# Optimization experiments

Measured on AMD Instinct MI355X. Metric: run time of the kernel, lower is better.

The kernel has to match this reference:

```python
import jax, jax.numpy as jnp
import numpy as np


def _chamfer(samp_pc, ref_pc):
    """Squared-L2 chamfer: returns (cost_p1_p2 [B,N], cost_p2_p1 [B,M]).

    samp_pc: [B, N, 3], ref_pc: [B, M, 3]
    """
    s2 = jnp.sum(samp_pc * samp_pc, axis=-1)  # [B, N]
    r2 = jnp.sum(ref_pc * ref_pc, axis=-1)    # [B, M]
    cross = jnp.einsum('bnd,bmd->bnm', samp_pc, ref_pc)  # [B, N, M]
    d2 = s2[:, :, None] + r2[:, None, :] - 2.0 * cross   # [B, N, M]
    d2 = jnp.maximum(d2, 0.0)  # numerical floor
    cost_p1_p2 = jnp.min(d2, axis=2)  # [B, N] nearest ref for each samp point
    cost_p2_p1 = jnp.min(d2, axis=1)  # [B, M] nearest samp for each ref point
    return cost_p1_p2, cost_p2_p1


def setup_inputs() -> dict:
    key = jax.random.key(0)
    k1, k2 = jax.random.split(key)
    B, N, M = 16, 2048, 8192
    ref_pc = jax.random.normal(k1, (B, M, 3), dtype=jnp.float32)
    samp_pc = jax.random.normal(k2, (B, N, 3), dtype=jnp.float32)
    return {"ref_pc": ref_pc, "samp_pc": samp_pc}


def reference(ref_pc, samp_pc):
    cost_p1_p2, cost_p2_p1 = _chamfer(samp_pc, ref_pc)
    cd_p = (jnp.sqrt(cost_p1_p2).mean(axis=1) + jnp.sqrt(cost_p2_p1).mean(axis=1)) / 2.0
    cd_t = cost_p1_p2.mean(axis=1) + cost_p2_p1.mean(axis=1)
    return (cd_p, cd_t)
```

## Files before the change

kernel.cpp:

```cpp
#include <hip/hip_runtime.h>
#include <math.h>

#define BB 16
#define NN 2048
#define MM 8192

#define BLK 256
#define QSTG 512
#define NSTAGE (NN / QSTG)
#define CTS (QSTG / 32)

typedef __attribute__((ext_vector_type(8))) short short8;
typedef __attribute__((ext_vector_type(16))) float f32x16;

union U16 { uint4 u; short8 s; };

static __device__ __forceinline__ unsigned short f2bf(float f) {
    unsigned int u = __float_as_uint(f);
    unsigned int r = (u + 0x7FFFu + ((u >> 16) & 1u)) >> 16;
    return (unsigned short)r;
}
static __device__ __forceinline__ float bf2f(unsigned short h) {
    return __uint_as_float(((unsigned int)h) << 16);
}

static __device__ __forceinline__ void glds16(const uint4* g, uint4* l) {
    __builtin_amdgcn_global_load_lds(
        (const __attribute__((address_space(1))) unsigned int*)g,
        (__attribute__((address_space(3))) unsigned int*)l,
        16, 0, 0);
}

#define DPP_MIN(v, CTRL)                                                      \
    v = fminf(v, __uint_as_float((unsigned)__builtin_amdgcn_update_dpp(       \
                     0, (int)__float_as_uint(v), CTRL, 0xF, 0xF, true)))
#define SWZ16_MIN(v)                                                          \
    v = fminf(v, __uint_as_float((unsigned)__builtin_amdgcn_ds_swizzle(       \
                     (int)__float_as_uint(v), 0x401F)))


__global__ void __launch_bounds__(BLK) prep_kernel(const float* __restrict__ ref,
                                                   const float* __restrict__ samp,
                                                   unsigned short* __restrict__ Qpk,
                                                   unsigned short* __restrict__ Rpk,
                                                   unsigned int* __restrict__ ws1) {
    const int i = blockIdx.x * BLK + threadIdx.x;
    const int PN = BB * NN;
    float a5[5];
    unsigned short h[3][5];
    unsigned short K[32];

    if (i < PN) {
        const float* s0 = samp + (size_t)i * 3;
        float x = s0[0], y = s0[1], z = s0[2];
        a5[0] = x; a5[1] = y; a5[2] = z;
        a5[3] = 1.f; a5[4] = fmaf(x, x, fmaf(y, y, z * z));
#pragma unroll
        for (int j = 0; j < 5; ++j) {
            float v = a5[j];
            h[0][j] = f2bf(v); float r1 = v - bf2f(h[0][j]);
            h[1][j] = f2bf(r1); float r2 = r1 - bf2f(h[1][j]);
            h[2][j] = f2bf(r2);
        }
        const int ordQ[6] = {0, 1, 0, 2, 0, 1};
#pragma unroll
        for (int f = 0; f < 2; ++f) {
#pragma unroll
            for (int p2 = 0; p2 < 3; ++p2)
#pragma unroll
                for (int j2 = 0; j2 < 5; ++j2)
                    K[f * 16 + p2 * 5 + j2] = h[ordQ[f * 3 + p2]][j2];
            K[f * 16 + 15] = 0;
        }
        unsigned int uu[16];
#pragma unroll
        for (int t = 0; t < 16; ++t)
            uu[t] = (unsigned int)K[2 * t] | ((unsigned int)K[2 * t + 1] << 16);
        uint4 c0 = make_uint4(uu[0], uu[1], uu[2], uu[3]);
        uint4 c1 = make_uint4(uu[4], uu[5], uu[6], uu[7]);
        uint4 c2 = make_uint4(uu[8], uu[9], uu[10], uu[11]);
        uint4 c3 = make_uint4(uu[12], uu[13], uu[14], uu[15]);
        uint4* dst = (uint4*)(Qpk + (size_t)i * 32);
        const int sw = (i >> 1) & 3;
        dst[0 ^ sw] = c0; dst[1 ^ sw] = c1; dst[2 ^ sw] = c2; dst[3 ^ sw] = c3;
        ws1[i] = 0x7F7F7F7Fu;
    } else if (i < PN + BB * MM) {
        const int j = i - PN;
        const float* r0 = ref + (size_t)j * 3;
        float x = r0[0], y = r0[1], z = r0[2];
        a5[0] = -2.f * x; a5[1] = -2.f * y; a5[2] = -2.f * z;
        a5[3] = fmaf(x, x, fmaf(y, y, z * z)); a5[4] = 1.f;
#pragma unroll
        for (int jj = 0; jj < 5; ++jj) {
            float v = a5[jj];
            h[0][jj] = f2bf(v); float r1 = v - bf2f(h[0][jj]);
            h[1][jj] = f2bf(r1); float r2 = r1 - bf2f(h[1][jj]);
            h[2][jj] = f2bf(r2);
        }
        const int ordR[6] = {0, 0, 1, 0, 2, 1};
#pragma unroll
        for (int f = 0; f < 2; ++f) {
#pragma unroll
            for (int p2 = 0; p2 < 3; ++p2)
#pragma unroll
                for (int j2 = 0; j2 < 5; ++j2)
                    K[f * 16 + p2 * 5 + j2] = h[ordR[f * 3 + p2]][j2];
            K[f * 16 + 15] = 0;
        }
        unsigned int uu[16];
#pragma unroll
        for (int t = 0; t < 16; ++t)
            uu[t] = (unsigned int)K[2 * t] | ((unsigned int)K[2 * t + 1] << 16);
        uint4* dst = (uint4*)(Rpk + (size_t)j * 32);
        dst[0] = make_uint4(uu[0], uu[1], uu[2], uu[3]);
        dst[1] = make_uint4(uu[4], uu[5], uu[6], uu[7]);
        dst[2] = make_uint4(uu[8], uu[9], uu[10], uu[11]);
        dst[3] = make_uint4(uu[12], uu[13], uu[14], uu[15]);
    }
}

__global__ void __launch_bounds__(BLK, 4) sweep_kernel(const unsigned short* __restrict__ Qpk,
                                                       const unsigned short* __restrict__ Rpk,
                                                       float* __restrict__ ws2,
                                                       unsigned int* __restrict__ ws1) {
    __shared__ uint4 Qt[2][QSTG * 4];
    __shared__ unsigned int qMin[NN];

    const int b = blockIdx.x;
    const int m0 = blockIdx.y * 256;
    const int tid = threadIdx.x;
    const int w = tid >> 6;
    const int l = tid & 63;
    const int p = l & 31;
    const int kh = l >> 5;

    const uint4* R4 = (const uint4*)Rpk + ((size_t)(b * MM + m0 + w * 64 + p)) * 4;
    U16 a0f0, a0f1, a1f0, a1f1;
    a0f0.u = R4[kh];        a0f1.u = R4[2 + kh];
    a1f0.u = R4[128 + kh];  a1f1.u = R4[128 + 2 + kh];

    for (int i = tid; i < NN; i += BLK) qMin[i] = 0x7F7F7F7Fu;

    const uint4* Q4 = (const uint4*)Qpk + (size_t)b * (NN * 4);
    {
        uint4* dst = &Qt[0][0];
#pragma unroll
        for (int k = 0; k < 8; ++k) glds16(Q4 + k * BLK + tid, dst + k * BLK + tid);
    }
    __syncthreads();

    float run0[16], run1[16];
#pragma unroll
    for (int j = 0; j < 16; ++j) { run0[j] = INFINITY; run1[j] = INFINITY; }

    const int sw = (p >> 1) & 3;
    const f32x16 fz = {0.f, 0.f, 0.f, 0.f, 0.f, 0.f, 0.f, 0.f,
                       0.f, 0.f, 0.f, 0.f, 0.f, 0.f, 0.f, 0.f};

    for (int st = 0; st < NSTAGE; ++st) {
        const uint4* qb = &Qt[st & 1][0];
        if (st < NSTAGE - 1) {
            const uint4* src = Q4 + (size_t)(st + 1) * (QSTG * 4);
            uint4* dst = &Qt[(st + 1) & 1][0];
#pragma unroll
            for (int k = 0; k < 8; ++k) glds16(src + k * BLK + tid, dst + k * BLK + tid);
        }
#pragma unroll 2
        for (int ct = 0; ct < CTS; ++ct) {
            const int pg = (ct * 32 + p) * 4;
            U16 b0, b1;
            b0.u = qb[pg + (kh ^ sw)];
            b1.u = qb[pg + ((2 + kh) ^ sw)];
            f32x16 d0 = __builtin_amdgcn_mfma_f32_32x32x16_bf16(a0f0.s, b0.s, fz, 0, 0, 0);
            d0 = __builtin_amdgcn_mfma_f32_32x32x16_bf16(a0f1.s, b1.s, d0, 0, 0, 0);
            f32x16 d1 = __builtin_amdgcn_mfma_f32_32x32x16_bf16(a1f0.s, b0.s, fz, 0, 0, 0);
            d1 = __builtin_amdgcn_mfma_f32_32x32x16_bf16(a1f1.s, b1.s, d1, 0, 0, 0);
#pragma unroll
            for (int j = 0; j < 16; ++j) {
                run0[j] = fminf(run0[j], d0[j]);
                run1[j] = fminf(run1[j], d1[j]);
            }
            float tv[8];
#pragma unroll
            for (int k = 0; k < 8; ++k) tv[k] = fminf(d0[k], d0[k + 8]);
#pragma unroll
            for (int k = 0; k < 8; ++k) tv[k] = fminf(tv[k], fminf(d1[k], d1[k + 8]));
#pragma unroll
            for (int k = 0; k < 4; ++k) tv[k] = fminf(tv[k], tv[k + 4]);
            float t = fminf(fminf(tv[0], tv[2]), fminf(tv[1], tv[3]));
            atomicMin(&qMin[st * QSTG + ct * 32 + p], __float_as_uint(fmaxf(t, 0.f)));
        }
        __syncthreads();
    }

#pragma unroll
    for (int i = tid; i < NN; i += BLK)
        atomicMin(&ws1[(size_t)b * NN + i], qMin[i]);

#pragma unroll
    for (int j = 0; j < 16; ++j) {
        DPP_MIN(run0[j], 0xB1);  DPP_MIN(run0[j], 0x4E);
        DPP_MIN(run0[j], 0x141); DPP_MIN(run0[j], 0x140);
        SWZ16_MIN(run0[j]);
        DPP_MIN(run1[j], 0xB1);  DPP_MIN(run1[j], 0x4E);
        DPP_MIN(run1[j], 0x141); DPP_MIN(run1[j], 0x140);
        SWZ16_MIN(run1[j]);
    }
    float out = 0.f;
#pragma unroll
    for (int j = 0; j < 16; ++j) { if (p == j)      out = run0[j]; }
#pragma unroll
    for (int j = 0; j < 16; ++j) { if (p == 16 + j) out = run1[j]; }
    const int t2 = p >> 4, j4 = p & 15;
    const int row = t2 * 32 + (j4 & 3) + ((j4 >> 2) << 3) + 4 * kh;
    ws2[(size_t)b * MM + m0 + w * 64 + row] = fmaxf(out, 0.f);
}

#define BLKR 1024
__global__ void __launch_bounds__(BLKR) reduce_kernel(const unsigned int* __restrict__ ws1,
                                                      const float* __restrict__ ws2,
                                                      float* __restrict__ out) {
    const int b = blockIdx.x;
    const int tid = threadIdx.x;
    const int lane = tid & 63;
    const int wv = tid >> 6;

    float sd1 = 0.f, sr1 = 0.f, sd2 = 0.f, sr2 = 0.f;
#pragma unroll
    for (int i = tid; i < NN; i += BLKR) {
        float v = __uint_as_float(ws1[(size_t)b * NN + i]);
        sd1 += v;
        sr1 += sqrtf(v);
    }
#pragma unroll
    for (int i = tid; i < MM; i += BLKR) {
        float v = ws2[(size_t)b * MM + i];
        sd2 += v;
        sr2 += sqrtf(v);
    }
#pragma unroll
    for (int s = 32; s > 0; s >>= 1) {
        sd1 += __shfl_xor(sd1, s);
        sr1 += __shfl_xor(sr1, s);
        sd2 += __shfl_xor(sd2, s);
        sr2 += __shfl_xor(sr2, s);
    }

    __shared__ float4 red[BLKR / 64];
    if (lane == 0) red[wv] = make_float4(sd1, sr1, sd2, sr2);
    __syncthreads();
    if (tid == 0) {
        float4 acc = red[0];
#pragma unroll
        for (int w = 1; w < BLKR / 64; ++w) {
            acc.x += red[w].x; acc.y += red[w].y;
            acc.z += red[w].z; acc.w += red[w].w;
        }
        out[b]      = (acc.y * (1.0f / NN) + acc.w * (1.0f / MM)) * 0.5f;
        out[BB + b] = acc.x * (1.0f / NN) + acc.z * (1.0f / MM);
    }
}

extern "C" void kernel_launch(void* const* d_in, const int* in_sizes, int n_in,
                              void* d_out, int out_size, void* d_ws, size_t ws_size,
                              hipStream_t stream) {
    const float* ref  = (const float*)d_in[0];
    const float* samp = (const float*)d_in[1];
    float* out = (float*)d_out;

    float* ws2 = (float*)d_ws;
    unsigned int* ws1 = (unsigned int*)(ws2 + (size_t)BB * MM);
    unsigned short* Qpk = (unsigned short*)(ws1 + (size_t)BB * NN);
    unsigned short* Rpk = Qpk + (size_t)BB * NN * 32;

    const int P = BB * (NN + MM);
    prep_kernel<<<P / BLK, BLK, 0, stream>>>(ref, samp, Qpk, Rpk, ws1);

    dim3 gs(BB, MM / 256);
    sweep_kernel<<<gs, BLK, 0, stream>>>(Qpk, Rpk, ws2, ws1);

    reduce_kernel<<<BB, BLKR, 0, stream>>>(ws1, ws2, out);
}
```

Baseline: 96.32 us.

## Split query dimension across blocks, fuse ref packing into sweep, drop global atomics

Adds a third grid dimension that splits the sample points into two halves, doubling the number of sweep blocks and halving the per-block LDS stage size. The reference-point bf16 packing moves from the prep kernel into the sweep kernel, where it is staged through shared memory. This removes the Rpk global round trip. Per-block column minima are written to a partial buffer instead of using global atomicMin, and the reduce kernel takes the min across the partials. The cost is more partial-buffer traffic in the reduce and redundant ref packing, since each of the two z-blocks repacks the same ref points.

Result: faster. 89.18 us (-7.4%).

```diff
diff --git a/kernel.cpp b/kernel.cpp
--- a/kernel.cpp
+++ b/kernel.cpp
@@ -6,9 +6,12 @@
 #define MM 8192
 
 #define BLK 256
-#define QSTG 512
-#define NSTAGE (NN / QSTG)
+#define QSPL 2
+#define NQ (NN / QSPL)
+#define QSTG 256
+#define NSTAGE (NQ / QSTG)
 #define CTS (QSTG / 32)
+#define YB (MM / 256)
 
 typedef __attribute__((ext_vector_type(8))) short short8;
 typedef __attribute__((ext_vector_type(16))) float f32x16;
@@ -39,22 +42,68 @@
                      (int)__float_as_uint(v), 0x401F)))
 
 
-__global__ void __launch_bounds__(BLK) prep_kernel(const float* __restrict__ ref,
-                                                   const float* __restrict__ samp,
-                                                   unsigned short* __restrict__ Qpk,
-                                                   unsigned short* __restrict__ Rpk,
-                                                   unsigned int* __restrict__ ws1) {
+__global__ void __launch_bounds__(BLK) prep_kernel(const float* __restrict__ samp,
+                                                   unsigned short* __restrict__ Qpk) {
     const int i = blockIdx.x * BLK + threadIdx.x;
-    const int PN = BB * NN;
+    const float* s0 = samp + (size_t)i * 3;
+    float x = s0[0], y = s0[1], z = s0[2];
     float a5[5];
+    a5[0] = x; a5[1] = y; a5[2] = z;
+    a5[3] = 1.f; a5[4] = fmaf(x, x, fmaf(y, y, z * z));
     unsigned short h[3][5];
+#pragma unroll
+    for (int j = 0; j < 5; ++j) {
+        float v = a5[j];
+        h[0][j] = f2bf(v); float r1 = v - bf2f(h[0][j]);
+        h[1][j] = f2bf(r1); float r2 = r1 - bf2f(h[1][j]);
+        h[2][j] = f2bf(r2);
+    }
+    const int ordQ[6] = {0, 1, 0, 2, 0, 1};
     unsigned short K[32];
-
-    if (i < PN) {
-        const float* s0 = samp + (size_t)i * 3;
-        float x = s0[0], y = s0[1], z = s0[2];
-        a5[0] = x; a5[1] = y; a5[2] = z;
-        a5[3] = 1.f; a5[4] = fmaf(x, x, fmaf(y, y, z * z));
+#pragma unroll
+    for (int f = 0; f < 2; ++f) {
+#pragma unroll
+        for (int p2 = 0; p2 < 3; ++p2)
+#pragma unroll
+            for (int j2 = 0; j2 < 5; ++j2)
+                K[f * 16 + p2 * 5 + j2] = h[ordQ[f * 3 + p2]][j2];
+        K[f * 16 + 15] = 0;
+    }
+    unsigned int uu[16];
+#pragma unroll
+    for (int t = 0; t < 16; ++t)
+        uu[t] = (unsigned int)K[2 * t] | ((unsigned int)K[2 * t + 1] << 16);
+    uint4* dst = (uint4*)(Qpk + (size_t)i * 32);
+    const int sw = (i >> 1) & 3;
+    dst[0 ^ sw] = make_uint4(uu[0], uu[1], uu[2], uu[3]);
+    dst[1 ^ sw] = make_uint4(uu[4], uu[5], uu[6], uu[7]);
+    dst[2 ^ sw] = make_uint4(uu[8], uu[9], uu[10], uu[11]);
+    dst[3 ^ sw] = make_uint4(uu[12], uu[13], uu[14], uu[15]);
+}
+
+__global__ void __launch_bounds__(BLK, 4) sweep_kernel(const float* __restrict__ ref,
+                                                       const unsigned short* __restrict__ Qpk,
+                                                       float* __restrict__ ws2p,
+                                                       float* __restrict__ ws1p) {
+    __shared__ uint4 Qt[2][QSTG * 4];
+    __shared__ unsigned int qMin[NQ];
+
+    const int b = blockIdx.x;
+    const int m0 = blockIdx.y * 256;
+    const int q0 = blockIdx.z * NQ;
+    const int tid = threadIdx.x;
+    const int w = tid >> 6;
+    const int l = tid & 63;
+    const int p = l & 31;
+    const int kh = l >> 5;
+
+    {
+        const float* r0 = ref + ((size_t)(b * MM + m0 + tid)) * 3;
+        float x = r0[0], y = r0[1], z = r0[2];
+        float a5[5];
+        a5[0] = -2.f * x; a5[1] = -2.f * y; a5[2] = -2.f * z;
+        a5[3] = fmaf(x, x, fmaf(y, y, z * z)); a5[4] = 1.f;
+        unsigned short h[3][5];
 #pragma unroll
         for (int j = 0; j < 5; ++j) {
             float v = a5[j];
@@ -62,42 +111,8 @@
             h[1][j] = f2bf(r1); float r2 = r1 - bf2f(h[1][j]);
             h[2][j] = f2bf(r2);
         }
-        const int ordQ[6] = {0, 1, 0, 2, 0, 1};
-#pragma unroll
-        for (int f = 0; f < 2; ++f) {
-#pragma unroll
-            for (int p2 = 0; p2 < 3; ++p2)
-#pragma unroll
-                for (int j2 = 0; j2 < 5; ++j2)
-                    K[f * 16 + p2 * 5 + j2] = h[ordQ[f * 3 + p2]][j2];
-            K[f * 16 + 15] = 0;
-        }
-        unsigned int uu[16];
-#pragma unroll
-        for (int t = 0; t < 16; ++t)
-            uu[t] = (unsigned int)K[2 * t] | ((unsigned int)K[2 * t + 1] << 16);
-        uint4 c0 = make_uint4(uu[0], uu[1], uu[2], uu[3]);
-        uint4 c1 = make_uint4(uu[4], uu[5], uu[6], uu[7]);
-        uint4 c2 = make_uint4(uu[8], uu[9], uu[10], uu[11]);
-        uint4 c3 = make_uint4(uu[12], uu[13], uu[14], uu[15]);
-        uint4* dst = (uint4*)(Qpk + (size_t)i * 32);
-        const int sw = (i >> 1) & 3;
-        dst[0 ^ sw] = c0; dst[1 ^ sw] = c1; dst[2 ^ sw] = c2; dst[3 ^ sw] = c3;
-        ws1[i] = 0x7F7F7F7Fu;
-    } else if (i < PN + BB * MM) {
-        const int j = i - PN;
-        const float* r0 = ref + (size_t)j * 3;
-        float x = r0[0], y = r0[1], z = r0[2];
-        a5[0] = -2.f * x; a5[1] = -2.f * y; a5[2] = -2.f * z;
-        a5[3] = fmaf(x, x, fmaf(y, y, z * z)); a5[4] = 1.f;
-#pragma unroll
-        for (int jj = 0; jj < 5; ++jj) {
-            float v = a5[jj];
-            h[0][jj] = f2bf(v); float r1 = v - bf2f(h[0][jj]);
-            h[1][jj] = f2bf(r1); float r2 = r1 - bf2f(h[1][jj]);
-            h[2][jj] = f2bf(r2);
-        }
         const int ordR[6] = {0, 0, 1, 0, 2, 1};
+        unsigned short K[32];
 #pragma unroll
         for (int f = 0; f < 2; ++f) {
 #pragma unroll
@@ -111,41 +126,29 @@
 #pragma unroll
         for (int t = 0; t < 16; ++t)
             uu[t] = (unsigned int)K[2 * t] | ((unsigned int)K[2 * t + 1] << 16);
-        uint4* dst = (uint4*)(Rpk + (size_t)j * 32);
-        dst[0] = make_uint4(uu[0], uu[1], uu[2], uu[3]);
-        dst[1] = make_uint4(uu[4], uu[5], uu[6], uu[7]);
-        dst[2] = make_uint4(uu[8], uu[9], uu[10], uu[11]);
-        dst[3] = make_uint4(uu[12], uu[13], uu[14], uu[15]);
-    }
-}
-
-__global__ void __launch_bounds__(BLK, 4) sweep_kernel(const unsigned short* __restrict__ Qpk,
-                                                       const unsigned short* __restrict__ Rpk,
-                                                       float* __restrict__ ws2,
-                                                       unsigned int* __restrict__ ws1) {
-    __shared__ uint4 Qt[2][QSTG * 4];
-    __shared__ unsigned int qMin[NN];
-
-    const int b = blockIdx.x;
-    const int m0 = blockIdx.y * 256;
-    const int tid = threadIdx.x;
-    const int w = tid >> 6;
-    const int l = tid & 63;
-    const int p = l & 31;
-    const int kh = l >> 5;
-
-    const uint4* R4 = (const uint4*)Rpk + ((size_t)(b * MM + m0 + w * 64 + p)) * 4;
+        uint4* scr = &Qt[1][0];
+        scr[0 * 256 + tid] = make_uint4(uu[0], uu[1], uu[2], uu[3]);
+        scr[1 * 256 + tid] = make_uint4(uu[4], uu[5], uu[6], uu[7]);
+        scr[2 * 256 + tid] = make_uint4(uu[8], uu[9], uu[10], uu[11]);
+        scr[3 * 256 + tid] = make_uint4(uu[12], uu[13], uu[14], uu[15]);
+    }
+    for (int i = tid; i < NQ; i += BLK) qMin[i] = 0x7F7F7F7Fu;
+    __syncthreads();
+
     U16 a0f0, a0f1, a1f0, a1f1;
-    a0f0.u = R4[kh];        a0f1.u = R4[2 + kh];
-    a1f0.u = R4[128 + kh];  a1f1.u = R4[128 + 2 + kh];
-
-    for (int i = tid; i < NN; i += BLK) qMin[i] = 0x7F7F7F7Fu;
-
-    const uint4* Q4 = (const uint4*)Qpk + (size_t)b * (NN * 4);
+    {
+        const uint4* scr = &Qt[1][0];
+        a0f0.u = scr[kh * 256 + w * 64 + p];
+        a0f1.u = scr[(2 + kh) * 256 + w * 64 + p];
+        a1f0.u = scr[kh * 256 + w * 64 + 32 + p];
+        a1f1.u = scr[(2 + kh) * 256 + w * 64 + 32 + p];
+    }
+
+    const uint4* Q4 = (const uint4*)Qpk + ((size_t)b * NN + q0) * 4;
     {
         uint4* dst = &Qt[0][0];
 #pragma unroll
-        for (int k = 0; k < 8; ++k) glds16(Q4 + k * BLK + tid, dst + k * BLK + tid);
+        for (int k = 0; k < 4; ++k) glds16(Q4 + k * BLK + tid, dst + k * BLK + tid);
     }
     __syncthreads();
 
@@ -163,7 +166,7 @@
             const uint4* src = Q4 + (size_t)(st + 1) * (QSTG * 4);
             uint4* dst = &Qt[(st + 1) & 1][0];
 #pragma unroll
-            for (int k = 0; k < 8; ++k) glds16(src + k * BLK + tid, dst + k * BLK + tid);
+            for (int k = 0; k < 4; ++k) glds16(src + k * BLK + tid, dst + k * BLK + tid);
         }
 #pragma unroll 2
         for (int ct = 0; ct < CTS; ++ct) {
@@ -193,9 +196,10 @@
         __syncthreads();
     }
 
-#pragma unroll
-    for (int i = tid; i < NN; i += BLK)
-        atomicMin(&ws1[(size_t)b * NN + i], qMin[i]);
+    float* w1 = ws1p + ((size_t)blockIdx.y * BB + b) * NN + q0;
+#pragma unroll
+    for (int i = tid; i < NQ; i += BLK)
+        w1[i] = __uint_as_float(qMin[i]);
 
 #pragma unroll
     for (int j = 0; j < 16; ++j) {
@@ -213,12 +217,12 @@
     for (int j = 0; j < 16; ++j) { if (p == 16 + j) out = run1[j]; }
     const int t2 = p >> 4, j4 = p & 15;
     const int row = t2 * 32 + (j4 & 3) + ((j4 >> 2) << 3) + 4 * kh;
-    ws2[(size_t)b * MM + m0 + w * 64 + row] = fmaxf(out, 0.f);
+    ws2p[((size_t)blockIdx.z * BB + b) * MM + m0 + w * 64 + row] = fmaxf(out, 0.f);
 }
 
 #define BLKR 1024
-__global__ void __launch_bounds__(BLKR) reduce_kernel(const unsigned int* __restrict__ ws1,
-                                                      const float* __restrict__ ws2,
+__global__ void __launch_bounds__(BLKR) reduce_kernel(const float* __restrict__ ws1p,
+                                                      const float* __restrict__ ws2p,
                                                       float* __restrict__ out) {
     const int b = blockIdx.x;
     const int tid = threadIdx.x;
@@ -228,13 +232,17 @@
     float sd1 = 0.f, sr1 = 0.f, sd2 = 0.f, sr2 = 0.f;
 #pragma unroll
     for (int i = tid; i < NN; i += BLKR) {
-        float v = __uint_as_float(ws1[(size_t)b * NN + i]);
-        sd1 += v;
-        sr1 += sqrtf(v);
+        float m = INFINITY;
+#pragma unroll
+        for (int y = 0; y < YB; ++y)
+            m = fminf(m, ws1p[((size_t)y * BB + b) * NN + i]);
+        sd1 += m;
+        sr1 += sqrtf(m);
     }
 #pragma unroll
     for (int i = tid; i < MM; i += BLKR) {
-        float v = ws2[(size_t)b * MM + i];
+        float v = fminf(ws2p[(size_t)b * MM + i],
+                        ws2p[((size_t)BB + b) * MM + i]);
         sd2 += v;
         sr2 += sqrtf(v);
     }
@@ -268,16 +276,14 @@
     const float* samp = (const float*)d_in[1];
     float* out = (float*)d_out;
 
-    float* ws2 = (float*)d_ws;
-    unsigned int* ws1 = (unsigned int*)(ws2 + (size_t)BB * MM);
-    unsigned short* Qpk = (unsigned short*)(ws1 + (size_t)BB * NN);
-    unsigned short* Rpk = Qpk + (size_t)BB * NN * 32;
-
-    const int P = BB * (NN + MM);
-    prep_kernel<<<P / BLK, BLK, 0, stream>>>(ref, samp, Qpk, Rpk, ws1);
-
-    dim3 gs(BB, MM / 256);
-    sweep_kernel<<<gs, BLK, 0, stream>>>(Qpk, Rpk, ws2, ws1);
-
-    reduce_kernel<<<BB, BLKR, 0, stream>>>(ws1, ws2, out);
-}
+    float* ws2p = (float*)d_ws;
+    float* ws1p = ws2p + (size_t)QSPL * BB * MM;
+    unsigned short* Qpk = (unsigned short*)(ws1p + (size_t)YB * BB * NN);
+
+    prep_kernel<<<(BB * NN) / BLK, BLK, 0, stream>>>(samp, Qpk);
+
+    dim3 gs(BB, MM / 256, QSPL);
+    sweep_kernel<<<gs, BLK, 0, stream>>>(ref, Qpk, ws2p, ws1p);
+
+    reduce_kernel<<<BB, BLKR, 0, stream>>>(ws1p, ws2p, out);
+}
```
